# Kernel optimization log

Measured on AMD Instinct MI355X. Metric: run time of the kernel, lower is better.

Reference implementation:

```python
import jax, jax.numpy as jnp
import numpy as np

K = 31            # kernel_size
P = K // 2        # padding
EPS = 1e-05
STRENGTH = 1.0


def _box_filter(x):
    """31x31 mean box filter with zero padding, done as two separable 1D passes.
    Exactly equals F.conv2d(x, ones(K,K)/K^2, padding=P) since the box kernel
    is separable and padding is zero-fill."""
    kh = jnp.ones((1, 1, K, 1), x.dtype) / K  # vertical pass
    kw = jnp.ones((1, 1, 1, K), x.dtype) / K  # horizontal pass
    dn = jax.lax.conv_dimension_numbers(x.shape, kh.shape, ('NCHW', 'OIHW', 'NCHW'))
    x = jax.lax.conv_general_dilated(x, kh, (1, 1), [(P, P), (0, 0)], dimension_numbers=dn)
    x = jax.lax.conv_general_dilated(x, kw, (1, 1), [(0, 0), (P, P)], dimension_numbers=dn)
    return x


def setup_inputs() -> dict:
    key = jax.random.key(0)
    # (B, 1, H, W) image in [0, 1]
    x = jax.random.uniform(key, (32, 1, 1024, 1024), dtype=jnp.float32)
    return {"x": x}


def reference(x):
    local_mean = _box_filter(x)
    local_sq_mean = _box_filter(x * x)
    local_var = local_sq_mean - local_mean * local_mean
    local_std = jnp.sqrt(jnp.maximum(local_var, EPS))  # clamp(min=eps) then sqrt
    normalized = (x - local_mean) / (local_std + EPS)
    enhanced = jax.nn.sigmoid(normalized * 0.5)
    return x * (1.0 - STRENGTH) + enhanced * STRENGTH
```

## Files before the change

kernel.cpp:

```cpp
#include <hip/hip_runtime.h>
#include <math.h>


#define KSZ    31
#define PAD    15
#define IMG_H  1024
#define IMG_W  1024
#define SH     64
#define GP     4
#define NPH    (SH / GP)
#define NT     512
#define LROW   66
#define LBUF   (16 * LROW)
#define EPSV   1e-5f

#define LDS_BARRIER() do {                                   \
    asm volatile("s_waitcnt lgkmcnt(0)" ::: "memory");       \
    __builtin_amdgcn_s_barrier();                            \
} while (0)

__global__ __launch_bounds__(NT, 4)
void lcn_fused_kernel(const float* __restrict__ x, float* __restrict__ out) {
    const int cpx = gridDim.x >> 3;
    const int bid = (blockIdx.x & 7) * cpx + (blockIdx.x >> 3);

    const int chunk = bid & 15;
    const int b     = bid >> 4;
    const int y0    = chunk * SH;

    const float* img  = x   + (size_t)b * (IMG_H * IMG_W);
    float*       oimg = out + (size_t)b * (IMG_H * IMG_W);

    __shared__ float2 vbuf[2][GP][LBUF];

    const int t    = threadIdx.x;
    const int wave = t >> 6;
    const int lane = t & 63;

    if (t < 256) {
        const int s = t >> 5;
        const int k = t & 31;
        float2* vb = &vbuf[s >> 2][s & 3][0];
        if (k < 16) vb[k * LROW] = make_float2(0.f, 0.f);
        else        vb[(k - 16) * LROW + (LROW - 1)] = make_float2(0.f, 0.f);
    }

    const float inv = 1.0f / 961.0f;

    if (wave >= 4) {
        const int pt = t & 255;
        const int c0 = 4 * pt;

        const int iv  = c0 + 16;
        const int wp0 = ((iv    ) & 15) * LROW + ((iv    ) >> 4);
        const int wp1 = ((iv + 1) & 15) * LROW + ((iv + 1) >> 4);
        const int wp2 = ((iv + 2) & 15) * LROW + ((iv + 2) >> 4);
        const int wp3 = ((iv + 3) & 15) * LROW + ((iv + 3) >> 4);

        float vs0=0,vs1=0,vs2=0,vs3=0, vq0=0,vq1=0,vq2=0,vq3=0;
        for (int y = y0 - PAD; y <= y0 + PAD; ++y) {
            const int yc = max(y, 0);
            float4 v = *(const float4*)(img + (size_t)yc * IMG_W + c0);
            const float m = (y >= 0) ? 1.f : 0.f;
            v.x *= m; v.y *= m; v.z *= m; v.w *= m;
            vs0 += v.x; vq0 = fmaf(v.x, v.x, vq0);
            vs1 += v.y; vq1 = fmaf(v.y, v.y, vq1);
            vs2 += v.z; vq2 = fmaf(v.z, v.z, vq2);
            vs3 += v.w; vq3 = fmaf(v.w, v.w, vq3);
        }

        #pragma unroll
        for (int r = 0; r < GP; ++r) {
            vbuf[0][r][wp0] = make_float2(vs0, vq0);
            vbuf[0][r][wp1] = make_float2(vs1, vq1);
            vbuf[0][r][wp2] = make_float2(vs2, vq2);
            vbuf[0][r][wp3] = make_float2(vs3, vq3);
            const int ys  = y0 + r - PAD;
            const int ya  = y0 + r + PAD + 1;
            const int ysc = max(ys, 0);
            float4 vS = *(const float4*)(img + (size_t)ysc * IMG_W + c0);
            float4 vA = *(const float4*)(img + (size_t)ya  * IMG_W + c0);
            const float mS = (ys >= 0) ? 1.f : 0.f;
            float s0 = vS.x*mS, s1 = vS.y*mS, s2 = vS.z*mS, s3 = vS.w*mS;
            vs0 += vA.x - s0; vq0 = fmaf(vA.x, vA.x, vq0); vq0 = fmaf(-s0, s0, vq0);
            vs1 += vA.y - s1; vq1 = fmaf(vA.y, vA.y, vq1); vq1 = fmaf(-s1, s1, vq1);
            vs2 += vA.z - s2; vq2 = fmaf(vA.z, vA.z, vq2); vq2 = fmaf(-s2, s2, vq2);
            vs3 += vA.w - s3; vq3 = fmaf(vA.w, vA.w, vq3); vq3 = fmaf(-s3, s3, vq3);
        }

        float4 pfS[GP], pfA[GP];
        {
            const int base = y0 + GP;
            #pragma unroll
            for (int r = 0; r < GP; ++r) {
                const int ys = base + r - PAD;
                const int ya = base + r + PAD + 1;
                pfS[r] = *(const float4*)(img + (size_t)max(ys, 0) * IMG_W + c0);
                pfA[r] = *(const float4*)(img + (size_t)min(ya, IMG_H - 1) * IMG_W + c0);
            }
        }

        for (int p = 0; p < NPH; ++p) {
            LDS_BARRIER();
            if (p < NPH - 1) {
                const int base = y0 + GP * (p + 1);
                float2* dst = &vbuf[(p + 1) & 1][0][0];
                #pragma unroll
                for (int r = 0; r < GP; ++r) {
                    float2* d = dst + r * LBUF;
                    d[wp0] = make_float2(vs0, vq0);
                    d[wp1] = make_float2(vs1, vq1);
                    d[wp2] = make_float2(vs2, vq2);
                    d[wp3] = make_float2(vs3, vq3);
                    const int ys = base + r - PAD;
                    const int ya = base + r + PAD + 1;
                    const float mS = (ys >= 0)    ? 1.f : 0.f;
                    const float mA = (ya < IMG_H) ? 1.f : 0.f;
                    float s0 = pfS[r].x*mS, s1 = pfS[r].y*mS,
                          s2 = pfS[r].z*mS, s3 = pfS[r].w*mS;
                    float a0 = pfA[r].x*mA, a1 = pfA[r].y*mA,
                          a2 = pfA[r].z*mA, a3 = pfA[r].w*mA;
                    vs0 += a0 - s0; vq0 = fmaf(a0, a0, vq0); vq0 = fmaf(-s0, s0, vq0);
                    vs1 += a1 - s1; vq1 = fmaf(a1, a1, vq1); vq1 = fmaf(-s1, s1, vq1);
                    vs2 += a2 - s2; vq2 = fmaf(a2, a2, vq2); vq2 = fmaf(-s2, s2, vq2);
                    vs3 += a3 - s3; vq3 = fmaf(a3, a3, vq3); vq3 = fmaf(-s3, s3, vq3);
                }
                if (p < NPH - 2) {
                    const int base2 = y0 + GP * (p + 2);
                    #pragma unroll
                    for (int r = 0; r < GP; ++r) {
                        const int ys = base2 + r - PAD;
                        const int ya = base2 + r + PAD + 1;
                        pfS[r] = *(const float4*)(img + (size_t)max(ys, 0) * IMG_W + c0);
                        pfA[r] = *(const float4*)(img + (size_t)min(ya, IMG_H - 1) * IMG_W + c0);
                    }
                }
            }
        }
    } else {
        const int cbase = lane << 4;

        for (int p = 0; p < NPH; ++p) {
            LDS_BARRIER();
            const int row = y0 + GP * p + wave;

            const float* xr = img + (size_t)row * IMG_W + cbase;
            float4 xa = ((const float4*)xr)[0];
            float4 xb = ((const float4*)xr)[1];
            float4 xc = ((const float4*)xr)[2];
            float4 xd = ((const float4*)xr)[3];

            const float2* vr = &vbuf[p & 1][wave][lane];

            float hsA = 0.f, hqA = 0.f, hsB = 0.f, hqB = 0.f;
            #pragma unroll
            for (int s = 1; s <= 31; s += 2) {
                float2 va = vr[(s & 15) * LROW + (s >> 4)];
                hsA += va.x; hqA += va.y;
                if (s + 1 <= 31) {
                    float2 vb2 = vr[((s + 1) & 15) * LROW + ((s + 1) >> 4)];
                    hsB += vb2.x; hqB += vb2.y;
                }
            }
            float hs = hsA + hsB, hq = hqA + hqB;

            float xs[16] = { xa.x, xa.y, xa.z, xa.w,  xb.x, xb.y, xb.z, xb.w,
                             xc.x, xc.y, xc.z, xc.w,  xd.x, xd.y, xd.z, xd.w };
            float res[16];
            #pragma unroll
            for (int j = 0; j < 16; ++j) {
                if (j > 0) {
                    float2 va  = vr[((j - 1) & 15) * LROW + 2];
                    float2 vsu = vr[(j & 15) * LROW];
                    hs += va.x - vsu.x;
                    hq += va.y - vsu.y;
                }
                const float mean = hs * inv;
                const float var  = fmaf(-mean, mean, hq * inv);
                const float stdv = sqrtf(fmaxf(var, EPSV));
                const float norm = (xs[j] - mean) *
                                   __builtin_amdgcn_rcpf(stdv + EPSV);
                res[j] = __builtin_amdgcn_rcpf(1.0f + __expf(-0.5f * norm));
            }

            float* orow = oimg + (size_t)row * IMG_W + cbase;
            ((float4*)orow)[0] = make_float4(res[0],  res[1],  res[2],  res[3]);
            ((float4*)orow)[1] = make_float4(res[4],  res[5],  res[6],  res[7]);
            ((float4*)orow)[2] = make_float4(res[8],  res[9],  res[10], res[11]);
            ((float4*)orow)[3] = make_float4(res[12], res[13], res[14], res[15]);
        }
    }
}

extern "C" void kernel_launch(void* const* d_in, const int* in_sizes, int n_in,
                              void* d_out, int out_size, void* d_ws, size_t ws_size,
                              hipStream_t stream) {
    (void)n_in; (void)out_size; (void)d_ws; (void)ws_size;
    const float* x = (const float*)d_in[0];
    float* out = (float*)d_out;
    const int B = in_sizes[0] / (IMG_H * IMG_W);
    dim3 grid(B * (IMG_H / SH));
    lcn_fused_kernel<<<grid, NT, 0, stream>>>(x, out);
}
```

Baseline: 85.37 us.

## Replace per-row horizontal window summation with wave-level prefix scan in LDS

The horizontal pass no longer builds each lane's initial 31-tap sum from 31 LDS reads. Each lane now does a local 16-element prefix over its column sums, then a wave-wide shuffle scan. The resulting inclusive prefix sums are written back to LDS, padded with totals on the right edge, and each output's window sum is taken as the difference of two prefix values. This lowers LDS reads and serial adds per row, at the cost of shuffle steps, extra LDS writes and an explicit wait. Differencing large prefix sums may also lose some float precision.

```diff
diff --git a/kernel.cpp b/kernel.cpp
--- a/kernel.cpp
+++ b/kernel.cpp
@@ -150,31 +150,44 @@
             float4 xc = ((const float4*)xr)[2];
             float4 xd = ((const float4*)xr)[3];
 
-            const float2* vr = &vbuf[p & 1][wave][lane];
-
-            float hsA = 0.f, hqA = 0.f, hsB = 0.f, hqB = 0.f;
-            #pragma unroll
-            for (int s = 1; s <= 31; s += 2) {
-                float2 va = vr[(s & 15) * LROW + (s >> 4)];
-                hsA += va.x; hqA += va.y;
-                if (s + 1 <= 31) {
-                    float2 vb2 = vr[((s + 1) & 15) * LROW + ((s + 1) >> 4)];
-                    hsB += vb2.x; hqB += vb2.y;
-                }
-            }
-            float hs = hsA + hsB, hq = hqA + hqB;
+            float2* slot = &vbuf[p & 1][wave][0];
+            float2* vr   = slot + lane;
+
+            float2 v[16];
+            #pragma unroll
+            for (int j = 0; j < 16; ++j) v[j] = vr[j * LROW + 1];
+
+            #pragma unroll
+            for (int j = 1; j < 16; ++j) { v[j].x += v[j-1].x; v[j].y += v[j-1].y; }
+
+            float Ts = v[15].x, Tq = v[15].y;
+            #pragma unroll
+            for (int d = 1; d < 64; d <<= 1) {
+                float us = __shfl_up(Ts, d);
+                float uq = __shfl_up(Tq, d);
+                if (lane >= d) { Ts += us; Tq += uq; }
+            }
+            const float Bs = Ts - v[15].x;
+            const float Bq = Tq - v[15].y;
+
+            #pragma unroll
+            for (int j = 0; j < 16; ++j)
+                vr[j * LROW + 1] = make_float2(Bs + v[j].x, Bq + v[j].y);
+            const float TOTs = __shfl(Ts, 63);
+            const float TOTq = __shfl(Tq, 63);
+            if (lane < 16) slot[lane * LROW + (LROW - 1)] = make_float2(TOTs, TOTq);
+            asm volatile("s_waitcnt lgkmcnt(0)" ::: "memory");
+            __builtin_amdgcn_sched_barrier(0);
 
             float xs[16] = { xa.x, xa.y, xa.z, xa.w,  xb.x, xb.y, xb.z, xb.w,
                              xc.x, xc.y, xc.z, xc.w,  xd.x, xd.y, xd.z, xd.w };
             float res[16];
             #pragma unroll
             for (int j = 0; j < 16; ++j) {
-                if (j > 0) {
-                    float2 va  = vr[((j - 1) & 15) * LROW + 2];
-                    float2 vsu = vr[(j & 15) * LROW];
-                    hs += va.x - vsu.x;
-                    hq += va.y - vsu.y;
-                }
+                float2 hi = (j == 0) ? vr[15 * LROW + 1] : vr[(j - 1) * LROW + 2];
+                float2 lo = vr[j * LROW];
+                const float hs = hi.x - lo.x;
+                const float hq = hi.y - lo.y;
                 const float mean = hs * inv;
                 const float var  = fmaf(-mean, mean, hq * inv);
                 const float stdv = sqrtf(fmaxf(var, EPSV));
```

Measured after the change: 89.28 us. 1.05x slower.

## Split image width into two column tiles with halo producers and smaller blocks

Applied to the files above, without the earlier changes.

Each block now handles a 64-row by 512-column tile instead of a full-width strip, so the grid doubles and the block shrinks from 512 to 320 threads. 136 producer threads compute vertical running sums over the tile plus a 16-column halo on each side, with masking at the image edges, and 2 consumer waves each cover two rows per phase. The LDS buffer halves and the launch bound asks for 5 blocks per CU, aiming at more resident blocks and better load balance. The sqrt-plus-reciprocal is also replaced by rsq with a first-order epsilon correction. In exchange, halo columns are read twice and producer waves are only partly filled.

```diff
diff --git a/kernel.cpp b/kernel.cpp
--- a/kernel.cpp
+++ b/kernel.cpp
@@ -7,11 +7,13 @@
 #define IMG_H  1024
 #define IMG_W  1024
 #define SH     64
+#define CW     512
 #define GP     4
 #define NPH    (SH / GP)
-#define NT     512
-#define LROW   66
-#define LBUF   (16 * LROW)
+#define NT     320
+#define NPROD  136
+#define LROW   34
+#define SLOT   (16 * LROW)
 #define EPSV   1e-5f
 
 #define LDS_BARRIER() do {                                   \
@@ -19,49 +21,47 @@
     __builtin_amdgcn_s_barrier();                            \
 } while (0)
 
-__global__ __launch_bounds__(NT, 4)
+__global__ __launch_bounds__(NT, 5)
 void lcn_fused_kernel(const float* __restrict__ x, float* __restrict__ out) {
     const int cpx = gridDim.x >> 3;
     const int bid = (blockIdx.x & 7) * cpx + (blockIdx.x >> 3);
 
-    const int chunk = bid & 15;
-    const int b     = bid >> 4;
-    const int y0    = chunk * SH;
+    const int xc = bid & 1;
+    const int yc = (bid >> 1) & 15;
+    const int b  = bid >> 5;
+    const int y0 = yc * SH;
+    const int x0 = xc * CW;
 
     const float* img  = x   + (size_t)b * (IMG_H * IMG_W);
     float*       oimg = out + (size_t)b * (IMG_H * IMG_W);
 
-    __shared__ float2 vbuf[2][GP][LBUF];
-
-    const int t    = threadIdx.x;
-    const int wave = t >> 6;
-    const int lane = t & 63;
-
-    if (t < 256) {
-        const int s = t >> 5;
-        const int k = t & 31;
-        float2* vb = &vbuf[s >> 2][s & 3][0];
-        if (k < 16) vb[k * LROW] = make_float2(0.f, 0.f);
-        else        vb[(k - 16) * LROW + (LROW - 1)] = make_float2(0.f, 0.f);
-    }
-
+    __shared__ float2 vbuf[2][GP][SLOT];
+
+    const int t = threadIdx.x;
+    const bool is_prod = (t < NPROD);
+    const bool is_cons = (t >= 192);
     const float inv = 1.0f / 961.0f;
 
-    if (wave >= 4) {
-        const int pt = t & 255;
-        const int c0 = 4 * pt;
-
-        const int iv  = c0 + 16;
-        const int wp0 = ((iv    ) & 15) * LROW + ((iv    ) >> 4);
-        const int wp1 = ((iv + 1) & 15) * LROW + ((iv + 1) >> 4);
-        const int wp2 = ((iv + 2) & 15) * LROW + ((iv + 2) >> 4);
-        const int wp3 = ((iv + 3) & 15) * LROW + ((iv + 3) >> 4);
-
-        float vs0=0,vs1=0,vs2=0,vs3=0, vq0=0,vq1=0,vq2=0,vq3=0;
+    float vs0=0,vs1=0,vs2=0,vs3=0, vq0=0,vq1=0,vq2=0,vq3=0;
+    float4 pfS[GP], pfA[GP];
+    int wp0=0, wp1=0, wp2=0, wp3=0, ga=0;
+    float cmf = 0.f;
+
+    if (is_prod) {
+        const int gc0 = x0 - 16 + 4 * t;
+        const bool cm = (gc0 >= 0) && (gc0 < IMG_W);
+        ga  = cm ? gc0 : 0;
+        cmf = cm ? 1.f : 0.f;
+        const int iv = 4 * t;
+        wp0 = ((iv    ) & 15) * LROW + ((iv    ) >> 4);
+        wp1 = ((iv + 1) & 15) * LROW + ((iv + 1) >> 4);
+        wp2 = ((iv + 2) & 15) * LROW + ((iv + 2) >> 4);
+        wp3 = ((iv + 3) & 15) * LROW + ((iv + 3) >> 4);
+
         for (int y = y0 - PAD; y <= y0 + PAD; ++y) {
-            const int yc = max(y, 0);
-            float4 v = *(const float4*)(img + (size_t)yc * IMG_W + c0);
-            const float m = (y >= 0) ? 1.f : 0.f;
+            const int ycl = max(y, 0);
+            float4 v = *(const float4*)(img + (size_t)ycl * IMG_W + ga);
+            const float m = ((y >= 0) ? 1.f : 0.f) * cmf;
             v.x *= m; v.y *= m; v.z *= m; v.w *= m;
             vs0 += v.x; vq0 = fmaf(v.x, v.x, vq0);
             vs1 += v.y; vq1 = fmaf(v.y, v.y, vq1);
@@ -78,44 +78,52 @@
             const int ys  = y0 + r - PAD;
             const int ya  = y0 + r + PAD + 1;
             const int ysc = max(ys, 0);
-            float4 vS = *(const float4*)(img + (size_t)ysc * IMG_W + c0);
-            float4 vA = *(const float4*)(img + (size_t)ya  * IMG_W + c0);
-            const float mS = (ys >= 0) ? 1.f : 0.f;
+            float4 vS = *(const float4*)(img + (size_t)ysc * IMG_W + ga);
+            float4 vA = *(const float4*)(img + (size_t)ya  * IMG_W + ga);
+            const float mS = ((ys >= 0) ? 1.f : 0.f) * cmf;
             float s0 = vS.x*mS, s1 = vS.y*mS, s2 = vS.z*mS, s3 = vS.w*mS;
-            vs0 += vA.x - s0; vq0 = fmaf(vA.x, vA.x, vq0); vq0 = fmaf(-s0, s0, vq0);
-            vs1 += vA.y - s1; vq1 = fmaf(vA.y, vA.y, vq1); vq1 = fmaf(-s1, s1, vq1);
-            vs2 += vA.z - s2; vq2 = fmaf(vA.z, vA.z, vq2); vq2 = fmaf(-s2, s2, vq2);
-            vs3 += vA.w - s3; vq3 = fmaf(vA.w, vA.w, vq3); vq3 = fmaf(-s3, s3, vq3);
-        }
-
-        float4 pfS[GP], pfA[GP];
+            float a0 = vA.x*cmf, a1 = vA.y*cmf, a2 = vA.z*cmf, a3 = vA.w*cmf;
+            vs0 += a0 - s0; vq0 = fmaf(a0, a0, vq0); vq0 = fmaf(-s0, s0, vq0);
+            vs1 += a1 - s1; vq1 = fmaf(a1, a1, vq1); vq1 = fmaf(-s1, s1, vq1);
+            vs2 += a2 - s2; vq2 = fmaf(a2, a2, vq2); vq2 = fmaf(-s2, s2, vq2);
+            vs3 += a3 - s3; vq3 = fmaf(a3, a3, vq3); vq3 = fmaf(-s3, s3, vq3);
+        }
+
         {
             const int base = y0 + GP;
             #pragma unroll
             for (int r = 0; r < GP; ++r) {
                 const int ys = base + r - PAD;
                 const int ya = base + r + PAD + 1;
-                pfS[r] = *(const float4*)(img + (size_t)max(ys, 0) * IMG_W + c0);
-                pfA[r] = *(const float4*)(img + (size_t)min(ya, IMG_H - 1) * IMG_W + c0);
-            }
-        }
-
-        for (int p = 0; p < NPH; ++p) {
-            LDS_BARRIER();
+                pfS[r] = *(const float4*)(img + (size_t)max(ys, 0) * IMG_W + ga);
+                pfA[r] = *(const float4*)(img + (size_t)min(ya, IMG_H - 1) * IMG_W + ga);
+            }
+        }
+    }
+
+    const int lane = t & 63;
+    const int cw   = (t >> 6) - 3;
+    const int rsub = lane >> 5;
+    const int lcol = (lane & 31) << 4;
+
+    for (int p = 0; p < NPH; ++p) {
+        LDS_BARRIER();
+
+        if (is_prod) {
             if (p < NPH - 1) {
                 const int base = y0 + GP * (p + 1);
                 float2* dst = &vbuf[(p + 1) & 1][0][0];
                 #pragma unroll
                 for (int r = 0; r < GP; ++r) {
-                    float2* d = dst + r * LBUF;
+                    float2* d = dst + r * SLOT;
                     d[wp0] = make_float2(vs0, vq0);
                     d[wp1] = make_float2(vs1, vq1);
                     d[wp2] = make_float2(vs2, vq2);
                     d[wp3] = make_float2(vs3, vq3);
                     const int ys = base + r - PAD;
                     const int ya = base + r + PAD + 1;
-                    const float mS = (ys >= 0)    ? 1.f : 0.f;
-                    const float mA = (ya < IMG_H) ? 1.f : 0.f;
+                    const float mS = ((ys >= 0)    ? 1.f : 0.f) * cmf;
+                    const float mA = ((ya < IMG_H) ? 1.f : 0.f) * cmf;
                     float s0 = pfS[r].x*mS, s1 = pfS[r].y*mS,
                           s2 = pfS[r].z*mS, s3 = pfS[r].w*mS;
                     float a0 = pfA[r].x*mA, a1 = pfA[r].y*mA,
@@ -131,41 +139,31 @@
                     for (int r = 0; r < GP; ++r) {
                         const int ys = base2 + r - PAD;
                         const int ya = base2 + r + PAD + 1;
-                        pfS[r] = *(const float4*)(img + (size_t)max(ys, 0) * IMG_W + c0);
-                        pfA[r] = *(const float4*)(img + (size_t)min(ya, IMG_H - 1) * IMG_W + c0);
+                        pfS[r] = *(const float4*)(img + (size_t)max(ys, 0) * IMG_W + ga);
+                        pfA[r] = *(const float4*)(img + (size_t)min(ya, IMG_H - 1) * IMG_W + ga);
                     }
                 }
             }
-        }
-    } else {
-        const int cbase = lane << 4;
-
-        for (int p = 0; p < NPH; ++p) {
-            LDS_BARRIER();
-            const int row = y0 + GP * p + wave;
-
-            const float* xr = img + (size_t)row * IMG_W + cbase;
+        } else if (is_cons) {
+            const int r   = 2 * cw + rsub;
+            const int row = y0 + GP * p + r;
+
+            const float* xr = img + (size_t)row * IMG_W + x0 + lcol;
             float4 xa = ((const float4*)xr)[0];
             float4 xb = ((const float4*)xr)[1];
-            float4 xc = ((const float4*)xr)[2];
+            float4 xc2 = ((const float4*)xr)[2];
             float4 xd = ((const float4*)xr)[3];
 
-            const float2* vr = &vbuf[p & 1][wave][lane];
-
-            float hsA = 0.f, hqA = 0.f, hsB = 0.f, hqB = 0.f;
+            const float2* vr = &vbuf[p & 1][r][lane & 31];
+
+            float hs = 0.f, hq = 0.f;
             #pragma unroll
-            for (int s = 1; s <= 31; s += 2) {
-                float2 va = vr[(s & 15) * LROW + (s >> 4)];
-                hsA += va.x; hqA += va.y;
-                if (s + 1 <= 31) {
-                    float2 vb2 = vr[((s + 1) & 15) * LROW + ((s + 1) >> 4)];
-                    hsB += vb2.x; hqB += vb2.y;
-                }
-            }
-            float hs = hsA + hsB, hq = hqA + hqB;
-
+            for (int s = 1; s <= 31; ++s) {
+                float2 v = vr[(s & 15) * LROW + (s >> 4)];
+                hs += v.x; hq += v.y;
+            }
             float xs[16] = { xa.x, xa.y, xa.z, xa.w,  xb.x, xb.y, xb.z, xb.w,
-                             xc.x, xc.y, xc.z, xc.w,  xd.x, xd.y, xd.z, xd.w };
+                             xc2.x, xc2.y, xc2.z, xc2.w,  xd.x, xd.y, xd.z, xd.w };
             float res[16];
             #pragma unroll
             for (int j = 0; j < 16; ++j) {
@@ -177,13 +175,14 @@
                 }
                 const float mean = hs * inv;
                 const float var  = fmaf(-mean, mean, hq * inv);
-                const float stdv = sqrtf(fmaxf(var, EPSV));
-                const float norm = (xs[j] - mean) *
-                                   __builtin_amdgcn_rcpf(stdv + EPSV);
+                const float vc   = fmaxf(var, EPSV);
+                const float tr   = __builtin_amdgcn_rsqf(vc);
+                const float dinv = tr - (EPSV * tr) * tr;
+                const float norm = (xs[j] - mean) * dinv;
                 res[j] = __builtin_amdgcn_rcpf(1.0f + __expf(-0.5f * norm));
             }
 
-            float* orow = oimg + (size_t)row * IMG_W + cbase;
+            float* orow = oimg + (size_t)row * IMG_W + x0 + lcol;
             ((float4*)orow)[0] = make_float4(res[0],  res[1],  res[2],  res[3]);
             ((float4*)orow)[1] = make_float4(res[4],  res[5],  res[6],  res[7]);
             ((float4*)orow)[2] = make_float4(res[8],  res[9],  res[10], res[11]);
@@ -199,6 +198,6 @@
     const float* x = (const float*)d_in[0];
     float* out = (float*)d_out;
     const int B = in_sizes[0] / (IMG_H * IMG_W);
-    dim3 grid(B * (IMG_H / SH));
+    dim3 grid(B * (IMG_H / SH) * (IMG_W / CW));
     lcn_fused_kernel<<<grid, NT, 0, stream>>>(x, out);
 }
```

New measurement: 150.1 us. 1.76x slower.

## Use 1024-thread blocks with single-buffered LDS and two-barrier handoff

Applied to the files above, without the earlier changes.

Doubles the block to 1024 threads, with 8 consumer waves handling 8 rows per phase and 8 producer waves each computing vertical sums for 2 columns instead of 4. The double-buffered LDS ring becomes a single buffer, and a second barrier per phase keeps producers from overwriting rows the consumers are still reading. The aim is more parallel consumer work per phase and fewer phases per block. In exchange, producer and consumer phases now serialize instead of overlapping. The aggressive launch bound may also force register limits or spills.

```diff
diff --git a/kernel.cpp b/kernel.cpp
--- a/kernel.cpp
+++ b/kernel.cpp
@@ -7,9 +7,10 @@
 #define IMG_H  1024
 #define IMG_W  1024
 #define SH     64
-#define GP     4
+#define GP     8
 #define NPH    (SH / GP)
-#define NT     512
+#define NT     1024
+#define NCONS  512
 #define LROW   66
 #define LBUF   (16 * LROW)
 #define EPSV   1e-5f
@@ -19,7 +20,7 @@
     __builtin_amdgcn_s_barrier();                            \
 } while (0)
 
-__global__ __launch_bounds__(NT, 4)
+__global__ __launch_bounds__(NT, 8)
 void lcn_fused_kernel(const float* __restrict__ x, float* __restrict__ out) {
     const int cpx = gridDim.x >> 3;
     const int bid = (blockIdx.x & 7) * cpx + (blockIdx.x >> 3);
@@ -31,99 +32,76 @@
     const float* img  = x   + (size_t)b * (IMG_H * IMG_W);
     float*       oimg = out + (size_t)b * (IMG_H * IMG_W);
 
-    __shared__ float2 vbuf[2][GP][LBUF];
+    __shared__ float2 vbuf[GP][LBUF];
 
     const int t    = threadIdx.x;
     const int wave = t >> 6;
     const int lane = t & 63;
 
-    if (t < 256) {
-        const int s = t >> 5;
-        const int k = t & 31;
-        float2* vb = &vbuf[s >> 2][s & 3][0];
-        if (k < 16) vb[k * LROW] = make_float2(0.f, 0.f);
-        else        vb[(k - 16) * LROW + (LROW - 1)] = make_float2(0.f, 0.f);
-    }
-
     const float inv = 1.0f / 961.0f;
 
-    if (wave >= 4) {
-        const int pt = t & 255;
-        const int c0 = 4 * pt;
+    if (t >= NCONS) {
+        const int pt = t - NCONS;
+        const int c0 = 2 * pt;
 
         const int iv  = c0 + 16;
         const int wp0 = ((iv    ) & 15) * LROW + ((iv    ) >> 4);
         const int wp1 = ((iv + 1) & 15) * LROW + ((iv + 1) >> 4);
-        const int wp2 = ((iv + 2) & 15) * LROW + ((iv + 2) >> 4);
-        const int wp3 = ((iv + 3) & 15) * LROW + ((iv + 3) >> 4);
 
-        float vs0=0,vs1=0,vs2=0,vs3=0, vq0=0,vq1=0,vq2=0,vq3=0;
+        float vs0 = 0.f, vq0 = 0.f, vs1 = 0.f, vq1 = 0.f;
         for (int y = y0 - PAD; y <= y0 + PAD; ++y) {
             const int yc = max(y, 0);
-            float4 v = *(const float4*)(img + (size_t)yc * IMG_W + c0);
+            float2 v = *(const float2*)(img + (size_t)yc * IMG_W + c0);
             const float m = (y >= 0) ? 1.f : 0.f;
-            v.x *= m; v.y *= m; v.z *= m; v.w *= m;
+            v.x *= m; v.y *= m;
             vs0 += v.x; vq0 = fmaf(v.x, v.x, vq0);
             vs1 += v.y; vq1 = fmaf(v.y, v.y, vq1);
-            vs2 += v.z; vq2 = fmaf(v.z, v.z, vq2);
-            vs3 += v.w; vq3 = fmaf(v.w, v.w, vq3);
         }
 
         #pragma unroll
         for (int r = 0; r < GP; ++r) {
-            vbuf[0][r][wp0] = make_float2(vs0, vq0);
-            vbuf[0][r][wp1] = make_float2(vs1, vq1);
-            vbuf[0][r][wp2] = make_float2(vs2, vq2);
-            vbuf[0][r][wp3] = make_float2(vs3, vq3);
+            vbuf[r][wp0] = make_float2(vs0, vq0);
+            vbuf[r][wp1] = make_float2(vs1, vq1);
             const int ys  = y0 + r - PAD;
             const int ya  = y0 + r + PAD + 1;
             const int ysc = max(ys, 0);
-            float4 vS = *(const float4*)(img + (size_t)ysc * IMG_W + c0);
-            float4 vA = *(const float4*)(img + (size_t)ya  * IMG_W + c0);
+            float2 vS = *(const float2*)(img + (size_t)ysc * IMG_W + c0);
+            float2 vA = *(const float2*)(img + (size_t)ya  * IMG_W + c0);
             const float mS = (ys >= 0) ? 1.f : 0.f;
-            float s0 = vS.x*mS, s1 = vS.y*mS, s2 = vS.z*mS, s3 = vS.w*mS;
+            float s0 = vS.x * mS, s1 = vS.y * mS;
             vs0 += vA.x - s0; vq0 = fmaf(vA.x, vA.x, vq0); vq0 = fmaf(-s0, s0, vq0);
             vs1 += vA.y - s1; vq1 = fmaf(vA.y, vA.y, vq1); vq1 = fmaf(-s1, s1, vq1);
-            vs2 += vA.z - s2; vq2 = fmaf(vA.z, vA.z, vq2); vq2 = fmaf(-s2, s2, vq2);
-            vs3 += vA.w - s3; vq3 = fmaf(vA.w, vA.w, vq3); vq3 = fmaf(-s3, s3, vq3);
         }
 
-        float4 pfS[GP], pfA[GP];
+        float2 sbv[GP], adv[GP];
         {
             const int base = y0 + GP;
             #pragma unroll
             for (int r = 0; r < GP; ++r) {
                 const int ys = base + r - PAD;
                 const int ya = base + r + PAD + 1;
-                pfS[r] = *(const float4*)(img + (size_t)max(ys, 0) * IMG_W + c0);
-                pfA[r] = *(const float4*)(img + (size_t)min(ya, IMG_H - 1) * IMG_W + c0);
+                sbv[r] = *(const float2*)(img + (size_t)max(ys, 0) * IMG_W + c0);
+                adv[r] = *(const float2*)(img + (size_t)min(ya, IMG_H - 1) * IMG_W + c0);
             }
         }
 
         for (int p = 0; p < NPH; ++p) {
             LDS_BARRIER();
+            LDS_BARRIER();
             if (p < NPH - 1) {
                 const int base = y0 + GP * (p + 1);
-                float2* dst = &vbuf[(p + 1) & 1][0][0];
                 #pragma unroll
                 for (int r = 0; r < GP; ++r) {
-                    float2* d = dst + r * LBUF;
-                    d[wp0] = make_float2(vs0, vq0);
-                    d[wp1] = make_float2(vs1, vq1);
-                    d[wp2] = make_float2(vs2, vq2);
-                    d[wp3] = make_float2(vs3, vq3);
+                    vbuf[r][wp0] = make_float2(vs0, vq0);
+                    vbuf[r][wp1] = make_float2(vs1, vq1);
                     const int ys = base + r - PAD;
                     const int ya = base + r + PAD + 1;
                     const float mS = (ys >= 0)    ? 1.f : 0.f;
                     const float mA = (ya < IMG_H) ? 1.f : 0.f;
-                    float s0 = pfS[r].x*mS, s1 = pfS[r].y*mS,
-                          s2 = pfS[r].z*mS, s3 = pfS[r].w*mS;
-                    float a0 = pfA[r].x*mA, a1 = pfA[r].y*mA,
-                          a2 = pfA[r].z*mA, a3 = pfA[r].w*mA;
+                    float s0 = sbv[r].x * mS, s1 = sbv[r].y * mS;
+                    float a0 = adv[r].x * mA, a1 = adv[r].y * mA;
                     vs0 += a0 - s0; vq0 = fmaf(a0, a0, vq0); vq0 = fmaf(-s0, s0, vq0);
                     vs1 += a1 - s1; vq1 = fmaf(a1, a1, vq1); vq1 = fmaf(-s1, s1, vq1);
-                    vs2 += a2 - s2; vq2 = fmaf(a2, a2, vq2); vq2 = fmaf(-s2, s2, vq2);
-                    vs3 += a3 - s3; vq3 = fmaf(a3, a3, vq3); vq3 = fmaf(-s3, s3, vq3);
                 }
                 if (p < NPH - 2) {
                     const int base2 = y0 + GP * (p + 2);
@@ -131,14 +109,22 @@
                     for (int r = 0; r < GP; ++r) {
                         const int ys = base2 + r - PAD;
                         const int ya = base2 + r + PAD + 1;
-                        pfS[r] = *(const float4*)(img + (size_t)max(ys, 0) * IMG_W + c0);
-                        pfA[r] = *(const float4*)(img + (size_t)min(ya, IMG_H - 1) * IMG_W + c0);
+                        sbv[r] = *(const float2*)(img + (size_t)max(ys, 0) * IMG_W + c0);
+                        adv[r] = *(const float2*)(img + (size_t)min(ya, IMG_H - 1) * IMG_W + c0);
                     }
                 }
             }
         }
     } else {
         const int cbase = lane << 4;
+
+        if (t < 256) {
+            const int s = t >> 5;
+            const int k = t & 31;
+            float2* vb = &vbuf[s][0];
+            if (k < 16) vb[k * LROW] = make_float2(0.f, 0.f);
+            else        vb[(k - 16) * LROW + (LROW - 1)] = make_float2(0.f, 0.f);
+        }
 
         for (int p = 0; p < NPH; ++p) {
             LDS_BARRIER();
@@ -150,7 +136,7 @@
             float4 xc = ((const float4*)xr)[2];
             float4 xd = ((const float4*)xr)[3];
 
-            const float2* vr = &vbuf[p & 1][wave][lane];
+            const float2* vr = &vbuf[wave][lane];
 
             float hsA = 0.f, hqA = 0.f, hsB = 0.f, hqB = 0.f;
             #pragma unroll
@@ -188,6 +174,8 @@
             ((float4*)orow)[1] = make_float4(res[4],  res[5],  res[6],  res[7]);
             ((float4*)orow)[2] = make_float4(res[8],  res[9],  res[10], res[11]);
             ((float4*)orow)[3] = make_float4(res[12], res[13], res[14], res[15]);
+
+            LDS_BARRIER();
         }
     }
 }
```

After: 96.87 us. 13.5% more time.
